# Performance work log

Measured on AMD Instinct MI355X. Metric: run time of the kernel, lower is better.

The kernel has to match this reference:

```python
import jax, jax.numpy as jnp
import numpy as np

N = 50000      # nodes
E = 800000     # edges (before self loops)
IN = 128       # in_channels
HID = 64       # hidden_channels
HEADS = 4
NCLS = 2
NEG_SLOPE = 0.2
BN_EPS = 1e-5

# per-layer config: (in_dim, heads, out_c, concat)
LAYERS = [(IN, HEADS, HID, True), (HID*HEADS, HEADS, HID, True), (HID*HEADS, HEADS, HID, True), (HID*HEADS, 1, HID, False)]

def setup_inputs():
    key = jax.random.key(0)
    ks = iter(jax.random.split(key, 64))
    d = {}
    d['x'] = jax.random.normal(next(ks), (N, IN), dtype=jnp.float32)
    d['edge_index'] = jax.random.randint(next(ks), (2, E), 0, N, dtype=jnp.int64)
    for i, (inc, h, oc, concat) in enumerate(LAYERS):
        d[f'W{i}'] = jax.random.normal(next(ks), (inc, h*oc), dtype=jnp.float32) * (1.0/np.sqrt(inc))
        d[f'as{i}'] = jax.random.normal(next(ks), (h, oc), dtype=jnp.float32) * 0.1
        d[f'ad{i}'] = jax.random.normal(next(ks), (h, oc), dtype=jnp.float32) * 0.1
        bn_dim = h*oc if concat else oc
        d[f'b{i}'] = jnp.zeros((bn_dim,), dtype=jnp.float32)
        d[f'g{i}'] = jnp.ones((bn_dim,), dtype=jnp.float32)
        d[f'be{i}'] = jnp.zeros((bn_dim,), dtype=jnp.float32)
    d['hw1'] = jax.random.normal(next(ks), (HID, HID//2), dtype=jnp.float32) * (1.0/np.sqrt(HID))
    d['hb1'] = jnp.zeros((HID//2,), dtype=jnp.float32)
    d['hw2'] = jax.random.normal(next(ks), (HID//2, NCLS), dtype=jnp.float32) * (1.0/np.sqrt(HID//2))
    d['hb2'] = jnp.zeros((NCLS,), dtype=jnp.float32)
    return d

def _gat_layer(x, src, dst, W, a_src, a_dst, bias, heads, out_c, concat):
    n = x.shape[0]
    h = (x @ W).reshape(n, heads, out_c)                 # [N,H,C]
    asrc = jnp.einsum('nhc,hc->nh', h, a_src)            # [N,H]
    adst = jnp.einsum('nhc,hc->nh', h, a_dst)            # [N,H]
    e = asrc[src] + adst[dst]                            # [Etot,H]
    e = jax.nn.leaky_relu(e, NEG_SLOPE)
    # segment softmax over incoming edges of each dst node
    m = jax.ops.segment_max(e, dst, num_segments=n)
    m = jnp.where(jnp.isfinite(m), m, 0.0)
    ex = jnp.exp(e - m[dst])
    s = jax.ops.segment_sum(ex, dst, num_segments=n)
    alpha = ex / (s[dst] + 1e-16)                        # [Etot,H]
    msg = h[src] * alpha[:, :, None]                     # [Etot,H,C]
    out = jax.ops.segment_sum(msg, dst, num_segments=n)  # [N,H,C]
    out = out.reshape(n, heads*out_c) if concat else out.mean(axis=1)
    return out + bias

def _bn(x, g, b):
    mu = x.mean(axis=0)
    var = x.var(axis=0)
    return g * (x - mu) * jax.lax.rsqrt(var + BN_EPS) + b

def reference(x, edge_index,
              W0, as0, ad0, b0, g0, be0,
              W1, as1, ad1, b1, g1, be1,
              W2, as2, ad2, b2, g2, be2,
              W3, as3, ad3, b3, g3, be3,
              hw1, hb1, hw2, hb2):
    loop = jnp.arange(N, dtype=edge_index.dtype)
    src = jnp.concatenate([edge_index[0], loop])
    dst = jnp.concatenate([edge_index[1], loop])
    params = [(W0, as0, ad0, b0, g0, be0), (W1, as1, ad1, b1, g1, be1),
              (W2, as2, ad2, b2, g2, be2), (W3, as3, ad3, b3, g3, be3)]
    h = x
    for (inc, heads, oc, concat), (W, a_s, a_d, b, g, be) in zip(LAYERS, params):
        h = _gat_layer(h, src, dst, W, a_s, a_d, b, heads, oc, concat)
        h = _bn(h, g, be)
        h = jax.nn.relu(h)
    h = jax.nn.relu(h @ hw1 + hb1)
    return h @ hw2 + hb2
```

## Files before the change

kernel.cpp:

```cpp
#include <hip/hip_runtime.h>

__device__ __forceinline__ float bf2f(unsigned short u) {
    union { unsigned int i; float f; } x;
    x.i = ((unsigned int)u) << 16;
    return x.f;
}
__device__ __forceinline__ unsigned short f2bf(float f) {
    union { float f; unsigned int i; } x;
    x.f = f;
    unsigned int r = x.i + 0x7fffu + ((x.i >> 16) & 1u);
    return (unsigned short)(r >> 16);
}
__device__ __forceinline__ float ldf(const void* p, int i, int f32m) {
    if (f32m) return ((const float*)p)[i];
    return bf2f(((const unsigned short*)p)[i]);
}
__device__ __forceinline__ void unpack2(unsigned int u, float& lo, float& hi) {
    union { unsigned int i; float f; } a, b;
    a.i = u << 16;
    b.i = u & 0xffff0000u;
    lo = a.f;
    hi = b.f;
}

__global__ void GATModel_20117626814707_kernel(unsigned short* out, int n) {
    int i = blockIdx.x * 256 + threadIdx.x;
    if (i < n) out[i] = f2bf(100.0f);
}

__global__ void zero_kernel(int* p, int n) {
    int i = blockIdx.x * 256 + threadIdx.x;
    if (i < n) p[i] = 0;
}

__global__ void probe_kernel(const int* ei, const unsigned int* xw, int* meta) {
    if (threadIdx.x == 0 && blockIdx.x == 0) {
        int orv = 0;
        for (int k = 0; k < 64; k++) orv |= ei[2 * k + 1];
        meta[0] = (orv == 0) ? 1 : 0;
        int cnt = 0;
        for (int k = 0; k < 64; k++) {
            unsigned int w = xw[k];
            int e = (int)((w >> 23) & 0xffu);
            if (e >= 107 && e <= 140) cnt++;
        }
        meta[1] = (cnt >= 48) ? 1 : 0;
    }
}

__global__ void hist_kernel(const int* ei, const int* meta, int* cnt, int E, int N) {
    int e = blockIdx.x * 256 + threadIdx.x;
    if (e >= E) return;
    int d = meta[0] ? ei[2 * (E + e)] : ei[E + e];
    if ((unsigned)d >= (unsigned)N) d = 0;
    atomicAdd(&cnt[d], 1);
}

__global__ void __launch_bounds__(1024) scan_kernel(const int* cnt, int* offs, int N) {
    __shared__ int part[1024];
    int tid = threadIdx.x;
    int per = (N + 1023) >> 10;
    int b = tid * per;
    int e_ = b + per;
    if (e_ > N) e_ = N;
    if (b > N) b = N;
    int s = 0;
    for (int i = b; i < e_; i++) s += cnt[i];
    part[tid] = s;
    __syncthreads();
    for (int off = 1; off < 1024; off <<= 1) {
        int t = (tid >= off) ? part[tid - off] : 0;
        __syncthreads();
        part[tid] += t;
        __syncthreads();
    }
    int run = part[tid] - s;
    for (int i = b; i < e_; i++) { offs[i] = run; run += cnt[i]; }
    if (tid == 1023) offs[N] = part[1023];
}

__global__ void scatter_kernel(const int* ei, const int* meta, const int* offs,
                               int* fill, int* csr, int E, int N) {
    int e = blockIdx.x * 256 + threadIdx.x;
    if (e >= E) return;
    int is64 = meta[0];
    int sv = is64 ? ei[2 * e] : ei[e];
    int d  = is64 ? ei[2 * (E + e)] : ei[E + e];
    if ((unsigned)sv >= (unsigned)N) sv = 0;
    if ((unsigned)d  >= (unsigned)N) d  = 0;
    int pos = offs[d] + atomicAdd(&fill[d], 1);
    csr[pos] = sv;
}

__global__ void __launch_bounds__(256) gemm_tiled(const void* Aptr, int a_is_input,
                                                  const void* Bptr, void* Cout, int out_bf16,
                                                  const void* aw_s, const void* aw_d,
                                                  float* asrc, float* adst,
                                                  int M, int K, int NC, const int* meta,
                                                  const float* bnscale, const float* bnshift,
                                                  int apply_bn) {
    __shared__ float At[32][68];
    __shared__ float Bt[32][64];
    int wmode = meta[1];
    int amode = a_is_input ? wmode : 1;
    int t = threadIdx.x;
    int row0 = blockIdx.x * 64;
    int col0 = blockIdx.y * 64;
    int H = NC >> 6;

    int tx = t & 15;
    int ty = t >> 4;

    int ar = t >> 2;
    int ak = (t & 3) * 8;
    int bk = t >> 3;
    int bc = (t & 7) * 8;

    float acc[4][4];
    #pragma unroll
    for (int i = 0; i < 4; i++)
        #pragma unroll
        for (int j = 0; j < 4; j++) acc[i][j] = 0.0f;

    for (int kt = 0; kt < K; kt += 32) {
        {
            int gr = row0 + ar;
            float av[8];
            if (gr < M) {
                if (amode) {
                    const float* ap = (const float*)Aptr + (size_t)gr * K + kt + ak;
                    float4 v0 = *(const float4*)ap;
                    float4 v1 = *(const float4*)(ap + 4);
                    av[0] = v0.x; av[1] = v0.y; av[2] = v0.z; av[3] = v0.w;
                    av[4] = v1.x; av[5] = v1.y; av[6] = v1.z; av[7] = v1.w;
                    if (apply_bn) {
                        float4 sc0 = *(const float4*)(bnscale + kt + ak);
                        float4 sc1 = *(const float4*)(bnscale + kt + ak + 4);
                        float4 sh0 = *(const float4*)(bnshift + kt + ak);
                        float4 sh1 = *(const float4*)(bnshift + kt + ak + 4);
                        av[0] = fmaxf(fmaf(av[0], sc0.x, sh0.x), 0.0f);
                        av[1] = fmaxf(fmaf(av[1], sc0.y, sh0.y), 0.0f);
                        av[2] = fmaxf(fmaf(av[2], sc0.z, sh0.z), 0.0f);
                        av[3] = fmaxf(fmaf(av[3], sc0.w, sh0.w), 0.0f);
                        av[4] = fmaxf(fmaf(av[4], sc1.x, sh1.x), 0.0f);
                        av[5] = fmaxf(fmaf(av[5], sc1.y, sh1.y), 0.0f);
                        av[6] = fmaxf(fmaf(av[6], sc1.z, sh1.z), 0.0f);
                        av[7] = fmaxf(fmaf(av[7], sc1.w, sh1.w), 0.0f);
                    }
                } else {
                    const unsigned short* ap =
                        (const unsigned short*)Aptr + (size_t)gr * K + kt + ak;
                    uint4 u = *(const uint4*)ap;
                    unpack2(u.x, av[0], av[1]);
                    unpack2(u.y, av[2], av[3]);
                    unpack2(u.z, av[4], av[5]);
                    unpack2(u.w, av[6], av[7]);
                }
            } else {
                #pragma unroll
                for (int i = 0; i < 8; i++) av[i] = 0.0f;
            }
            #pragma unroll
            for (int i = 0; i < 8; i++) At[ak + i][ar] = av[i];
        }
        {
            if (wmode) {
                const float* bp = (const float*)Bptr + (size_t)(kt + bk) * NC + col0 + bc;
                *(float4*)&Bt[bk][bc] = *(const float4*)bp;
                *(float4*)&Bt[bk][bc + 4] = *(const float4*)(bp + 4);
            } else {
                const unsigned short* bp =
                    (const unsigned short*)Bptr + (size_t)(kt + bk) * NC + col0 + bc;
                uint4 u = *(const uint4*)bp;
                float4 v0, v1;
                unpack2(u.x, v0.x, v0.y);
                unpack2(u.y, v0.z, v0.w);
                unpack2(u.z, v1.x, v1.y);
                unpack2(u.w, v1.z, v1.w);
                *(float4*)&Bt[bk][bc] = v0;
                *(float4*)&Bt[bk][bc + 4] = v1;
            }
        }
        __syncthreads();

        #pragma unroll
        for (int k = 0; k < 32; k++) {
            float4 a = *(float4*)&At[k][ty * 4];
            float4 b = *(float4*)&Bt[k][tx * 4];
            acc[0][0] = fmaf(a.x, b.x, acc[0][0]);
            acc[0][1] = fmaf(a.x, b.y, acc[0][1]);
            acc[0][2] = fmaf(a.x, b.z, acc[0][2]);
            acc[0][3] = fmaf(a.x, b.w, acc[0][3]);
            acc[1][0] = fmaf(a.y, b.x, acc[1][0]);
            acc[1][1] = fmaf(a.y, b.y, acc[1][1]);
            acc[1][2] = fmaf(a.y, b.z, acc[1][2]);
            acc[1][3] = fmaf(a.y, b.w, acc[1][3]);
            acc[2][0] = fmaf(a.z, b.x, acc[2][0]);
            acc[2][1] = fmaf(a.z, b.y, acc[2][1]);
            acc[2][2] = fmaf(a.z, b.z, acc[2][2]);
            acc[2][3] = fmaf(a.z, b.w, acc[2][3]);
            acc[3][0] = fmaf(a.w, b.x, acc[3][0]);
            acc[3][1] = fmaf(a.w, b.y, acc[3][1]);
            acc[3][2] = fmaf(a.w, b.z, acc[3][2]);
            acc[3][3] = fmaf(a.w, b.w, acc[3][3]);
        }
        __syncthreads();
    }

    #pragma unroll
    for (int i = 0; i < 4; i++) {
        int gr = row0 + ty * 4 + i;
        if (gr < M) {
            if (out_bf16) {
                uint2 v;
                v.x = (unsigned int)f2bf(acc[i][0]) | ((unsigned int)f2bf(acc[i][1]) << 16);
                v.y = (unsigned int)f2bf(acc[i][2]) | ((unsigned int)f2bf(acc[i][3]) << 16);
                *(uint2*)&((unsigned short*)Cout)[(size_t)gr * NC + col0 + tx * 4] = v;
            } else {
                float4 v;
                v.x = acc[i][0]; v.y = acc[i][1]; v.z = acc[i][2]; v.w = acc[i][3];
                *(float4*)&((float*)Cout)[(size_t)gr * NC + col0 + tx * 4] = v;
            }
        }
    }

    int ai = blockIdx.y * 64 + tx * 4;
    float as0 = ldf(aw_s, ai + 0, wmode), as1 = ldf(aw_s, ai + 1, wmode);
    float as2 = ldf(aw_s, ai + 2, wmode), as3 = ldf(aw_s, ai + 3, wmode);
    float ad0 = ldf(aw_d, ai + 0, wmode), ad1 = ldf(aw_d, ai + 1, wmode);
    float ad2 = ldf(aw_d, ai + 2, wmode), ad3 = ldf(aw_d, ai + 3, wmode);
    #pragma unroll
    for (int i = 0; i < 4; i++) {
        float ps = acc[i][0] * as0 + acc[i][1] * as1 + acc[i][2] * as2 + acc[i][3] * as3;
        float pd = acc[i][0] * ad0 + acc[i][1] * ad1 + acc[i][2] * ad2 + acc[i][3] * ad3;
        #pragma unroll
        for (int off = 1; off < 16; off <<= 1) {
            ps += __shfl_xor(ps, off);
            pd += __shfl_xor(pd, off);
        }
        int gr = row0 + ty * 4 + i;
        if (tx == 0 && gr < M) {
            asrc[gr * H + blockIdx.y] = ps;
            adst[gr * H + blockIdx.y] = pd;
        }
    }
}

__global__ void __launch_bounds__(256) aggb4(const unsigned short* hfb, const float* asrc,
                                             const float* adst, const int* offs,
                                             const int* csr, float* out, int N) {
    int wid = threadIdx.x >> 6;
    int l = threadIdx.x & 63;
    int node = blockIdx.x * 4 + wid;
    if (node >= N) return;
    int h = l >> 4;
    int beg = offs[node], end = offs[node + 1];
    float ad = adst[node * 4 + h];
    float e0 = asrc[node * 4 + h] + ad;
    e0 = (e0 < 0.0f) ? 0.2f * e0 : e0;
    float w0 = __expf(e0);
    uint2 u0 = ((const uint2*)(hfb + (size_t)node * 256))[l];
    float g0a, g0b, g0c, g0d;
    unpack2(u0.x, g0a, g0b);
    unpack2(u0.y, g0c, g0d);
    float s = w0;
    float a0 = w0 * g0a, a1 = w0 * g0b, a2 = w0 * g0c, a3 = w0 * g0d;
    int i = beg;
    for (; i + 4 <= end; i += 4) {
        int s0 = csr[i], s1 = csr[i + 1], s2 = csr[i + 2], s3 = csr[i + 3];
        float e_0 = asrc[s0 * 4 + h] + ad;
        float e_1 = asrc[s1 * 4 + h] + ad;
        float e_2 = asrc[s2 * 4 + h] + ad;
        float e_3 = asrc[s3 * 4 + h] + ad;
        uint2 u_0 = ((const uint2*)(hfb + (size_t)s0 * 256))[l];
        uint2 u_1 = ((const uint2*)(hfb + (size_t)s1 * 256))[l];
        uint2 u_2 = ((const uint2*)(hfb + (size_t)s2 * 256))[l];
        uint2 u_3 = ((const uint2*)(hfb + (size_t)s3 * 256))[l];
        e_0 = (e_0 < 0.0f) ? 0.2f * e_0 : e_0;
        e_1 = (e_1 < 0.0f) ? 0.2f * e_1 : e_1;
        e_2 = (e_2 < 0.0f) ? 0.2f * e_2 : e_2;
        e_3 = (e_3 < 0.0f) ? 0.2f * e_3 : e_3;
        float wv0 = __expf(e_0), wv1 = __expf(e_1), wv2 = __expf(e_2), wv3 = __expf(e_3);
        s += (wv0 + wv1) + (wv2 + wv3);
        float x0, x1, x2, x3;
        unpack2(u_0.x, x0, x1); unpack2(u_0.y, x2, x3);
        a0 = fmaf(wv0, x0, a0); a1 = fmaf(wv0, x1, a1);
        a2 = fmaf(wv0, x2, a2); a3 = fmaf(wv0, x3, a3);
        unpack2(u_1.x, x0, x1); unpack2(u_1.y, x2, x3);
        a0 = fmaf(wv1, x0, a0); a1 = fmaf(wv1, x1, a1);
        a2 = fmaf(wv1, x2, a2); a3 = fmaf(wv1, x3, a3);
        unpack2(u_2.x, x0, x1); unpack2(u_2.y, x2, x3);
        a0 = fmaf(wv2, x0, a0); a1 = fmaf(wv2, x1, a1);
        a2 = fmaf(wv2, x2, a2); a3 = fmaf(wv2, x3, a3);
        unpack2(u_3.x, x0, x1); unpack2(u_3.y, x2, x3);
        a0 = fmaf(wv3, x0, a0); a1 = fmaf(wv3, x1, a1);
        a2 = fmaf(wv3, x2, a2); a3 = fmaf(wv3, x3, a3);
    }
    for (; i < end; i++) {
        int sn = csr[i];
        float es = asrc[sn * 4 + h] + ad;
        es = (es < 0.0f) ? 0.2f * es : es;
        float wv = __expf(es);
        uint2 u = ((const uint2*)(hfb + (size_t)sn * 256))[l];
        float x0, x1, x2, x3;
        unpack2(u.x, x0, x1); unpack2(u.y, x2, x3);
        s += wv;
        a0 = fmaf(wv, x0, a0); a1 = fmaf(wv, x1, a1);
        a2 = fmaf(wv, x2, a2); a3 = fmaf(wv, x3, a3);
    }
    float rs = 1.0f / (s + 1e-16f);
    float4 o;
    o.x = a0 * rs; o.y = a1 * rs; o.z = a2 * rs; o.w = a3 * rs;
    *(float4*)&out[(size_t)node * 256 + l * 4] = o;
}

__global__ void __launch_bounds__(256) aggf1(const float* hf, const float* asrc,
                                             const float* adst, const int* offs,
                                             const int* csr, float* out, int N) {
    int wid = threadIdx.x >> 6;
    int c = threadIdx.x & 63;
    int node = blockIdx.x * 4 + wid;
    if (node >= N) return;
    int beg = offs[node], end = offs[node + 1];
    float ad = adst[node];
    float e0 = asrc[node] + ad;
    e0 = (e0 < 0.0f) ? 0.2f * e0 : e0;
    float w0 = __expf(e0);
    float s = w0;
    float acc0 = w0 * hf[(size_t)node * 64 + c];
    float acc1 = 0.0f, acc2 = 0.0f, acc3 = 0.0f;
    int i = beg;
    for (; i + 4 <= end; i += 4) {
        int s0 = csr[i], s1 = csr[i + 1], s2 = csr[i + 2], s3 = csr[i + 3];
        float e_0 = asrc[s0] + ad;
        float e_1 = asrc[s1] + ad;
        float e_2 = asrc[s2] + ad;
        float e_3 = asrc[s3] + ad;
        float g0 = hf[(size_t)s0 * 64 + c];
        float g1 = hf[(size_t)s1 * 64 + c];
        float g2 = hf[(size_t)s2 * 64 + c];
        float g3 = hf[(size_t)s3 * 64 + c];
        e_0 = (e_0 < 0.0f) ? 0.2f * e_0 : e_0;
        e_1 = (e_1 < 0.0f) ? 0.2f * e_1 : e_1;
        e_2 = (e_2 < 0.0f) ? 0.2f * e_2 : e_2;
        e_3 = (e_3 < 0.0f) ? 0.2f * e_3 : e_3;
        float w0_ = __expf(e_0), w1_ = __expf(e_1), w2_ = __expf(e_2), w3_ = __expf(e_3);
        s += (w0_ + w1_) + (w2_ + w3_);
        acc0 = fmaf(w0_, g0, acc0);
        acc1 = fmaf(w1_, g1, acc1);
        acc2 = fmaf(w2_, g2, acc2);
        acc3 = fmaf(w3_, g3, acc3);
    }
    for (; i < end; i++) {
        int sn = csr[i];
        float es = asrc[sn] + ad;
        es = (es < 0.0f) ? 0.2f * es : es;
        float wv = __expf(es);
        s += wv;
        acc0 = fmaf(wv, hf[(size_t)sn * 64 + c], acc0);
    }
    float acc = (acc0 + acc1) + (acc2 + acc3);
    out[(size_t)node * 64 + c] = acc / (s + 1e-16f);
}

__global__ void __launch_bounds__(256) bnstats_kernel(const float* x, float* sum, float* sq,
                                                      int N, int NC, int ncshift) {
    int f = threadIdx.x & (NC - 1);
    int rsub = threadIdx.x >> ncshift;
    int rstep = 256 >> ncshift;
    int r0 = blockIdx.x * 256 + rsub;
    int r1 = blockIdx.x * 256 + 256;
    if (r1 > N) r1 = N;
    float s = 0.0f, q = 0.0f;
    for (int r = r0; r < r1; r += rstep) {
        float v = x[(size_t)r * NC + f];
        s += v;
        q += v * v;
    }
    atomicAdd(&sum[f], s);
    atomicAdd(&sq[f], q);
}

__global__ void bnfinal(const float* sum, const float* sq, const void* g, const void* be,
                        float* scale, float* shift, int NC, float invN, const int* meta) {
    int f = threadIdx.x;
    if (f >= NC) return;
    int wmode = meta[1];
    float mu = sum[f] * invN;
    float var = sq[f] * invN - mu * mu;
    if (var < 0.0f) var = 0.0f;
    float rs = rsqrtf(var + 1e-5f);
    float sc = ldf(g, f, wmode) * rs;
    scale[f] = sc;
    shift[f] = ldf(be, f, wmode) - mu * sc;
}

__global__ void __launch_bounds__(256) head_kernel(const float* xin, const float* bnscale,
                                                   const float* bnshift, const void* hw1,
                                                   const void* hb1, const void* hw2,
                                                   const void* hb2, void* out, int N,
                                                   const int* meta) {
    __shared__ float w1[64 * 32];
    __shared__ float w2[64];
    __shared__ float b1[32];
    __shared__ float b2[2];
    __shared__ float sc[64];
    __shared__ float sh[64];
    int wmode = meta[1];
    for (int i = threadIdx.x; i < 2048; i += 256) w1[i] = ldf(hw1, i, wmode);
    if (threadIdx.x < 64) {
        w2[threadIdx.x] = ldf(hw2, threadIdx.x, wmode);
        sc[threadIdx.x] = bnscale[threadIdx.x];
        sh[threadIdx.x] = bnshift[threadIdx.x];
    }
    if (threadIdx.x < 32) b1[threadIdx.x] = ldf(hb1, threadIdx.x, wmode);
    if (threadIdx.x < 2) b2[threadIdx.x] = ldf(hb2, threadIdx.x, wmode);
    __syncthreads();
    int n = blockIdx.x * 256 + threadIdx.x;
    if (n >= N) return;
    float x[64];
    for (int i = 0; i < 64; i++)
        x[i] = fmaxf(fmaf(xin[(size_t)n * 64 + i], sc[i], sh[i]), 0.0f);
    float o0 = b2[0], o1 = b2[1];
    for (int j = 0; j < 32; j++) {
        float a = b1[j];
        #pragma unroll
        for (int k = 0; k < 64; k++) a = fmaf(x[k], w1[k * 32 + j], a);
        a = fmaxf(a, 0.0f);
        o0 = fmaf(a, w2[j * 2], o0);
        o1 = fmaf(a, w2[j * 2 + 1], o1);
    }
    if (wmode) {
        ((float*)out)[n * 2] = o0;
        ((float*)out)[n * 2 + 1] = o1;
    } else {
        ((unsigned short*)out)[n * 2] = f2bf(o0);
        ((unsigned short*)out)[n * 2 + 1] = f2bf(o1);
    }
}

extern "C" void kernel_launch(void* const* d_in, const int* in_sizes, int n_in,
                              void* d_out, int out_size, void* d_ws, size_t ws_size,
                              hipStream_t stream) {
    unsigned short* outp = (unsigned short*)d_out;
    size_t out_bytes2 = (size_t)out_size * 2;
    int gOut = (out_size + 255) / 256;

    GATModel_20117626814707_kernel<<<gOut, 256, 0, stream>>>(outp, out_size);

    if (n_in != 30 || in_sizes[0] != 50000 * 128 || in_sizes[1] != 2 * 800000 ||
        in_sizes[2] != 128 * 256 || in_sizes[26] != 64 * 32) {
        hipMemsetAsync(d_out, 0x4E, out_bytes2, stream);
        return;
    }

    const int N = 50000;
    const int E = 800000;

    const void* x_in = d_in[0];
    const int* ei = (const int*)d_in[1];
    const void* W0  = d_in[2];
    const void* As0 = d_in[3];
    const void* Ad0 = d_in[4];
    const void* G0  = d_in[6];
    const void* Be0 = d_in[7];
    const void* W1  = d_in[8];
    const void* As1 = d_in[9];
    const void* Ad1 = d_in[10];
    const void* G1  = d_in[12];
    const void* Be1 = d_in[13];
    const void* W2  = d_in[14];
    const void* As2 = d_in[15];
    const void* Ad2 = d_in[16];
    const void* G2  = d_in[18];
    const void* Be2 = d_in[19];
    const void* W3  = d_in[20];
    const void* As3 = d_in[21];
    const void* Ad3 = d_in[22];
    const void* G3  = d_in[24];
    const void* Be3 = d_in[25];
    const void* hw1 = d_in[26];
    const void* hb1 = d_in[27];
    const void* hw2 = d_in[28];
    const void* hb2 = d_in[29];

    char* base = (char*)d_ws;
    size_t off = 0;
    auto alloc = [&](size_t bytes) {
        void* r = (void*)(base + off);
        off += (bytes + 255) & ~(size_t)255;
        return r;
    };
    int* meta    = (int*)alloc(256);
    int* cnt     = (int*)alloc((size_t)N * 4);
    int* fill    = (int*)alloc((size_t)N * 4);
    float* stats = (float*)alloc(4 * 2 * 256 * 4);
    size_t zero_end = off;
    int* offs    = (int*)alloc((size_t)(N + 1) * 4);
    int* csr     = (int*)alloc((size_t)E * 4);
    float* asrc  = (float*)alloc((size_t)N * 4 * 4);
    float* adst  = (float*)alloc((size_t)N * 4 * 4);
    float* scaleb = (float*)alloc(256 * 4);
    float* shiftb = (float*)alloc(256 * 4);
    unsigned short* hfb = (unsigned short*)alloc((size_t)N * 256 * 2);
    float* hff   = (float*)alloc((size_t)N * 64 * 4);
    float* xbuf  = (float*)alloc((size_t)N * 256 * 4);

    if (ws_size < off) {
        hipMemsetAsync(d_out, 0x4D, out_bytes2, stream);
        return;
    }

    int zn = (int)((zero_end - 256) / 4);
    zero_kernel<<<(zn + 255) / 256, 256, 0, stream>>>(cnt, zn);
    probe_kernel<<<1, 64, 0, stream>>>(ei, (const unsigned int*)x_in, meta);

    int gE = (E + 255) / 256;
    hist_kernel<<<gE, 256, 0, stream>>>(ei, meta, cnt, E, N);
    scan_kernel<<<1, 1024, 0, stream>>>(cnt, offs, N);
    scatter_kernel<<<gE, 256, 0, stream>>>(ei, meta, offs, fill, csr, E, N);

    int gM64 = (N + 63) / 64;
    int gBN = (N + 255) / 256;
    int gND = (N + 3) / 4;
    float invN = 1.0f / (float)N;

    const void* Wl[3]  = {W0, W1, W2};
    const void* Asl[3] = {As0, As1, As2};
    const void* Adl[3] = {Ad0, Ad1, Ad2};
    const void* Gl[3]  = {G0, G1, G2};
    const void* Bel[3] = {Be0, Be1, Be2};
    for (int L = 0; L < 3; L++) {
        if (L == 0)
            gemm_tiled<<<dim3(gM64, 4), 256, 0, stream>>>(
                x_in, 1, Wl[L], hfb, 1, Asl[L], Adl[L], asrc, adst, N, 128, 256, meta,
                scaleb, shiftb, 0);
        else
            gemm_tiled<<<dim3(gM64, 4), 256, 0, stream>>>(
                xbuf, 0, Wl[L], hfb, 1, Asl[L], Adl[L], asrc, adst, N, 256, 256, meta,
                scaleb, shiftb, 1);
        aggb4<<<gND, 256, 0, stream>>>(hfb, asrc, adst, offs, csr, xbuf, N);
        bnstats_kernel<<<gBN, 256, 0, stream>>>(xbuf, stats + L * 512, stats + L * 512 + 256, N, 256, 8);
        bnfinal<<<1, 256, 0, stream>>>(stats + L * 512, stats + L * 512 + 256, Gl[L], Bel[L],
                                       scaleb, shiftb, 256, invN, meta);
    }

    gemm_tiled<<<dim3(gM64, 1), 256, 0, stream>>>(
        xbuf, 0, W3, hff, 0, As3, Ad3, asrc, adst, N, 256, 64, meta, scaleb, shiftb, 1);
    aggf1<<<gND, 256, 0, stream>>>(hff, asrc, adst, offs, csr, xbuf, N);
    bnstats_kernel<<<gBN, 256, 0, stream>>>(xbuf, stats + 1536, stats + 1792, N, 64, 6);
    bnfinal<<<1, 256, 0, stream>>>(stats + 1536, stats + 1792, G3, Be3,
                                   scaleb, shiftb, 64, invN, meta);

    head_kernel<<<gBN, 256, 0, stream>>>(xbuf, scaleb, shiftb, hw1, hb1, hw2, hb2, d_out, N, meta);
}
```

Measured before the change: 1.075 ms.

## Replace FP32 SIMT GEMM with split-bf16 MFMA GEMM using hi/lo operand decomposition

The FP32 FMA tiled GEMM is replaced by a matrix-core kernel using bf16 MFMA 16x16x32 instructions. Accuracy is kept close to FP32 by splitting each operand into high and low bf16 parts and issuing three MFMAs (hi*hi, lo*hi, hi*lo). New pre-pass kernels split the activations, with BN+ReLU fused in, and transpose-split the weights. This adds extra memory passes for the split activation buffers and three MFMAs per tile.

```diff
diff --git a/kernel.cpp b/kernel.cpp
--- a/kernel.cpp
+++ b/kernel.cpp
@@ -1,4 +1,7 @@
 #include <hip/hip_runtime.h>
+
+typedef __attribute__((ext_vector_type(8))) short bf16x8;
+typedef __attribute__((ext_vector_type(4))) float f32x4;
 
 __device__ __forceinline__ float bf2f(unsigned short u) {
     union { unsigned int i; float f; } x;
@@ -92,156 +95,161 @@
     csr[pos] = sv;
 }
 
-__global__ void __launch_bounds__(256) gemm_tiled(const void* Aptr, int a_is_input,
-                                                  const void* Bptr, void* Cout, int out_bf16,
-                                                  const void* aw_s, const void* aw_d,
-                                                  float* asrc, float* adst,
-                                                  int M, int K, int NC, const int* meta,
-                                                  const float* bnscale, const float* bnshift,
-                                                  int apply_bn) {
-    __shared__ float At[32][68];
-    __shared__ float Bt[32][64];
+__global__ void __launch_bounds__(256) split_kernel(const void* X, int x_is_input,
+                                                    const int* meta, const float* scale,
+                                                    const float* shift, int apply_bn,
+                                                    unsigned short* hi, unsigned short* lo,
+                                                    int total4, int kmask) {
+    int idx = blockIdx.x * 256 + threadIdx.x;
+    if (idx >= total4) return;
+    int base = idx * 4;
+    int xmode = x_is_input ? meta[1] : 1;
+    float v[4];
+    if (xmode) {
+        float4 f = *(const float4*)((const float*)X + base);
+        v[0] = f.x; v[1] = f.y; v[2] = f.z; v[3] = f.w;
+    } else {
+        uint2 u = *(const uint2*)((const unsigned short*)X + base);
+        unpack2(u.x, v[0], v[1]);
+        unpack2(u.y, v[2], v[3]);
+    }
+    if (apply_bn) {
+        int f0 = base & kmask;
+        #pragma unroll
+        for (int j = 0; j < 4; j++)
+            v[j] = fmaxf(fmaf(v[j], scale[f0 + j], shift[f0 + j]), 0.0f);
+    }
+    unsigned short h[4], l[4];
+    #pragma unroll
+    for (int j = 0; j < 4; j++) {
+        h[j] = f2bf(v[j]);
+        l[j] = f2bf(v[j] - bf2f(h[j]));
+    }
+    uint2 ho, loo;
+    ho.x = (unsigned int)h[0] | ((unsigned int)h[1] << 16);
+    ho.y = (unsigned int)h[2] | ((unsigned int)h[3] << 16);
+    loo.x = (unsigned int)l[0] | ((unsigned int)l[1] << 16);
+    loo.y = (unsigned int)l[2] | ((unsigned int)l[3] << 16);
+    *(uint2*)(hi + base) = ho;
+    *(uint2*)(lo + base) = loo;
+}
+
+__global__ void __launch_bounds__(256) wsplit_kernel(const void* W, const int* meta,
+                                                     unsigned short* hiT, unsigned short* loT,
+                                                     int K, int ncshift, int total) {
+    int e = blockIdx.x * 256 + threadIdx.x;
+    if (e >= total) return;
+    int k = e >> ncshift;
+    int n = e & ((1 << ncshift) - 1);
+    float x = ldf(W, e, meta[1]);
+    unsigned short h = f2bf(x);
+    hiT[n * K + k] = h;
+    loT[n * K + k] = f2bf(x - bf2f(h));
+}
+
+__global__ void __launch_bounds__(256) gemm_mfma(const unsigned short* Ahi,
+                                                 const unsigned short* Alo,
+                                                 const unsigned short* Bhi,
+                                                 const unsigned short* Blo,
+                                                 void* Cout, int out_bf16,
+                                                 const void* aw_s, const void* aw_d,
+                                                 float* asrc, float* adst,
+                                                 int M, int K, int NC, const int* meta) {
+    __shared__ unsigned short sAhi[64 * 40];
+    __shared__ unsigned short sAlo[64 * 40];
+    __shared__ unsigned short sBhi[64 * 40];
+    __shared__ unsigned short sBlo[64 * 40];
     int wmode = meta[1];
-    int amode = a_is_input ? wmode : 1;
     int t = threadIdx.x;
+    int wid = t >> 6;
+    int lane = t & 63;
     int row0 = blockIdx.x * 64;
     int col0 = blockIdx.y * 64;
     int H = NC >> 6;
 
-    int tx = t & 15;
-    int ty = t >> 4;
-
     int ar = t >> 2;
     int ak = (t & 3) * 8;
-    int bk = t >> 3;
-    int bc = (t & 7) * 8;
-
-    float acc[4][4];
+
+    f32x4 acc[4];
     #pragma unroll
-    for (int i = 0; i < 4; i++)
-        #pragma unroll
-        for (int j = 0; j < 4; j++) acc[i][j] = 0.0f;
+    for (int i = 0; i < 4; i++) acc[i] = (f32x4){0.0f, 0.0f, 0.0f, 0.0f};
+
+    int m = lane & 15;
+    int q = lane >> 4;
 
     for (int kt = 0; kt < K; kt += 32) {
         {
             int gr = row0 + ar;
-            float av[8];
+            uint4 h4 = {0, 0, 0, 0}, l4 = {0, 0, 0, 0};
             if (gr < M) {
-                if (amode) {
-                    const float* ap = (const float*)Aptr + (size_t)gr * K + kt + ak;
-                    float4 v0 = *(const float4*)ap;
-                    float4 v1 = *(const float4*)(ap + 4);
-                    av[0] = v0.x; av[1] = v0.y; av[2] = v0.z; av[3] = v0.w;
-                    av[4] = v1.x; av[5] = v1.y; av[6] = v1.z; av[7] = v1.w;
-                    if (apply_bn) {
-                        float4 sc0 = *(const float4*)(bnscale + kt + ak);
-                        float4 sc1 = *(const float4*)(bnscale + kt + ak + 4);
-                        float4 sh0 = *(const float4*)(bnshift + kt + ak);
-                        float4 sh1 = *(const float4*)(bnshift + kt + ak + 4);
-                        av[0] = fmaxf(fmaf(av[0], sc0.x, sh0.x), 0.0f);
-                        av[1] = fmaxf(fmaf(av[1], sc0.y, sh0.y), 0.0f);
-                        av[2] = fmaxf(fmaf(av[2], sc0.z, sh0.z), 0.0f);
-                        av[3] = fmaxf(fmaf(av[3], sc0.w, sh0.w), 0.0f);
-                        av[4] = fmaxf(fmaf(av[4], sc1.x, sh1.x), 0.0f);
-                        av[5] = fmaxf(fmaf(av[5], sc1.y, sh1.y), 0.0f);
-                        av[6] = fmaxf(fmaf(av[6], sc1.z, sh1.z), 0.0f);
-                        av[7] = fmaxf(fmaf(av[7], sc1.w, sh1.w), 0.0f);
-                    }
-                } else {
-                    const unsigned short* ap =
-                        (const unsigned short*)Aptr + (size_t)gr * K + kt + ak;
-                    uint4 u = *(const uint4*)ap;
-                    unpack2(u.x, av[0], av[1]);
-                    unpack2(u.y, av[2], av[3]);
-                    unpack2(u.z, av[4], av[5]);
-                    unpack2(u.w, av[6], av[7]);
-                }
-            } else {
-                #pragma unroll
-                for (int i = 0; i < 8; i++) av[i] = 0.0f;
+                h4 = *(const uint4*)(Ahi + (size_t)gr * K + kt + ak);
+                l4 = *(const uint4*)(Alo + (size_t)gr * K + kt + ak);
             }
-            #pragma unroll
-            for (int i = 0; i < 8; i++) At[ak + i][ar] = av[i];
-        }
-        {
-            if (wmode) {
-                const float* bp = (const float*)Bptr + (size_t)(kt + bk) * NC + col0 + bc;
-                *(float4*)&Bt[bk][bc] = *(const float4*)bp;
-                *(float4*)&Bt[bk][bc + 4] = *(const float4*)(bp + 4);
-            } else {
-                const unsigned short* bp =
-                    (const unsigned short*)Bptr + (size_t)(kt + bk) * NC + col0 + bc;
-                uint4 u = *(const uint4*)bp;
-                float4 v0, v1;
-                unpack2(u.x, v0.x, v0.y);
-                unpack2(u.y, v0.z, v0.w);
-                unpack2(u.z, v1.x, v1.y);
-                unpack2(u.w, v1.z, v1.w);
-                *(float4*)&Bt[bk][bc] = v0;
-                *(float4*)&Bt[bk][bc + 4] = v1;
+            *(uint4*)(sAhi + ar * 40 + ak) = h4;
+            *(uint4*)(sAlo + ar * 40 + ak) = l4;
+            uint4 bh4 = *(const uint4*)(Bhi + (size_t)(col0 + ar) * K + kt + ak);
+            uint4 bl4 = *(const uint4*)(Blo + (size_t)(col0 + ar) * K + kt + ak);
+            *(uint4*)(sBhi + ar * 40 + ak) = bh4;
+            *(uint4*)(sBlo + ar * 40 + ak) = bl4;
+        }
+        __syncthreads();
+
+        bf16x8 ahi = *(const bf16x8*)(sAhi + (wid * 16 + m) * 40 + q * 8);
+        bf16x8 alo = *(const bf16x8*)(sAlo + (wid * 16 + m) * 40 + q * 8);
+        #pragma unroll
+        for (int tn = 0; tn < 4; tn++) {
+            bf16x8 bhi = *(const bf16x8*)(sBhi + (tn * 16 + m) * 40 + q * 8);
+            bf16x8 blo = *(const bf16x8*)(sBlo + (tn * 16 + m) * 40 + q * 8);
+            acc[tn] = __builtin_amdgcn_mfma_f32_16x16x32_bf16(ahi, bhi, acc[tn], 0, 0, 0);
+            acc[tn] = __builtin_amdgcn_mfma_f32_16x16x32_bf16(alo, bhi, acc[tn], 0, 0, 0);
+            acc[tn] = __builtin_amdgcn_mfma_f32_16x16x32_bf16(ahi, blo, acc[tn], 0, 0, 0);
+        }
+        __syncthreads();
+    }
+
+    #pragma unroll
+    for (int tn = 0; tn < 4; tn++) {
+        int gcol = col0 + tn * 16 + m;
+        #pragma unroll
+        for (int reg = 0; reg < 4; reg++) {
+            int grow = row0 + wid * 16 + q * 4 + reg;
+            if (grow < M) {
+                if (out_bf16)
+                    ((unsigned short*)Cout)[(size_t)grow * NC + gcol] = f2bf(acc[tn][reg]);
+                else
+                    ((float*)Cout)[(size_t)grow * NC + gcol] = acc[tn][reg];
             }
         }
-        __syncthreads();
-
-        #pragma unroll
-        for (int k = 0; k < 32; k++) {
-            float4 a = *(float4*)&At[k][ty * 4];
-            float4 b = *(float4*)&Bt[k][tx * 4];
-            acc[0][0] = fmaf(a.x, b.x, acc[0][0]);
-            acc[0][1] = fmaf(a.x, b.y, acc[0][1]);
-            acc[0][2] = fmaf(a.x, b.z, acc[0][2]);
-            acc[0][3] = fmaf(a.x, b.w, acc[0][3]);
-            acc[1][0] = fmaf(a.y, b.x, acc[1][0]);
-            acc[1][1] = fmaf(a.y, b.y, acc[1][1]);
-            acc[1][2] = fmaf(a.y, b.z, acc[1][2]);
-            acc[1][3] = fmaf(a.y, b.w, acc[1][3]);
-            acc[2][0] = fmaf(a.z, b.x, acc[2][0]);
-            acc[2][1] = fmaf(a.z, b.y, acc[2][1]);
-            acc[2][2] = fmaf(a.z, b.z, acc[2][2]);
-            acc[2][3] = fmaf(a.z, b.w, acc[2][3]);
-            acc[3][0] = fmaf(a.w, b.x, acc[3][0]);
-            acc[3][1] = fmaf(a.w, b.y, acc[3][1]);
-            acc[3][2] = fmaf(a.w, b.z, acc[3][2]);
-            acc[3][3] = fmaf(a.w, b.w, acc[3][3]);
-        }
-        __syncthreads();
-    }
-
+    }
+
+    float ps[4] = {0.f, 0.f, 0.f, 0.f};
+    float pd[4] = {0.f, 0.f, 0.f, 0.f};
     #pragma unroll
-    for (int i = 0; i < 4; i++) {
-        int gr = row0 + ty * 4 + i;
-        if (gr < M) {
-            if (out_bf16) {
-                uint2 v;
-                v.x = (unsigned int)f2bf(acc[i][0]) | ((unsigned int)f2bf(acc[i][1]) << 16);
-                v.y = (unsigned int)f2bf(acc[i][2]) | ((unsigned int)f2bf(acc[i][3]) << 16);
-                *(uint2*)&((unsigned short*)Cout)[(size_t)gr * NC + col0 + tx * 4] = v;
-            } else {
-                float4 v;
-                v.x = acc[i][0]; v.y = acc[i][1]; v.z = acc[i][2]; v.w = acc[i][3];
-                *(float4*)&((float*)Cout)[(size_t)gr * NC + col0 + tx * 4] = v;
+    for (int tn = 0; tn < 4; tn++) {
+        float asv = ldf(aw_s, blockIdx.y * 64 + tn * 16 + m, wmode);
+        float adv = ldf(aw_d, blockIdx.y * 64 + tn * 16 + m, wmode);
+        #pragma unroll
+        for (int reg = 0; reg < 4; reg++) {
+            ps[reg] = fmaf(acc[tn][reg], asv, ps[reg]);
+            pd[reg] = fmaf(acc[tn][reg], adv, pd[reg]);
+        }
+    }
+    #pragma unroll
+    for (int reg = 0; reg < 4; reg++) {
+        #pragma unroll
+        for (int off = 1; off < 16; off <<= 1) {
+            ps[reg] += __shfl_xor(ps[reg], off);
+            pd[reg] += __shfl_xor(pd[reg], off);
+        }
+    }
+    if (m == 0) {
+        #pragma unroll
+        for (int reg = 0; reg < 4; reg++) {
+            int grow = row0 + wid * 16 + q * 4 + reg;
+            if (grow < M) {
+                asrc[grow * H + blockIdx.y] = ps[reg];
+                adst[grow * H + blockIdx.y] = pd[reg];
             }
-        }
-    }
-
-    int ai = blockIdx.y * 64 + tx * 4;
-    float as0 = ldf(aw_s, ai + 0, wmode), as1 = ldf(aw_s, ai + 1, wmode);
-    float as2 = ldf(aw_s, ai + 2, wmode), as3 = ldf(aw_s, ai + 3, wmode);
-    float ad0 = ldf(aw_d, ai + 0, wmode), ad1 = ldf(aw_d, ai + 1, wmode);
-    float ad2 = ldf(aw_d, ai + 2, wmode), ad3 = ldf(aw_d, ai + 3, wmode);
-    #pragma unroll
-    for (int i = 0; i < 4; i++) {
-        float ps = acc[i][0] * as0 + acc[i][1] * as1 + acc[i][2] * as2 + acc[i][3] * as3;
-        float pd = acc[i][0] * ad0 + acc[i][1] * ad1 + acc[i][2] * ad2 + acc[i][3] * ad3;
-        #pragma unroll
-        for (int off = 1; off < 16; off <<= 1) {
-            ps += __shfl_xor(ps, off);
-            pd += __shfl_xor(pd, off);
-        }
-        int gr = row0 + ty * 4 + i;
-        if (tx == 0 && gr < M) {
-            asrc[gr * H + blockIdx.y] = ps;
-            adst[gr * H + blockIdx.y] = pd;
         }
     }
 }
@@ -505,6 +513,16 @@
     unsigned short* hfb = (unsigned short*)alloc((size_t)N * 256 * 2);
     float* hff   = (float*)alloc((size_t)N * 64 * 4);
     float* xbuf  = (float*)alloc((size_t)N * 256 * 4);
+    unsigned short* ahi = (unsigned short*)alloc((size_t)N * 256 * 2);
+    unsigned short* alo = (unsigned short*)alloc((size_t)N * 256 * 2);
+    unsigned short* w0hi = (unsigned short*)alloc(128 * 256 * 2);
+    unsigned short* w0lo = (unsigned short*)alloc(128 * 256 * 2);
+    unsigned short* w1hi = (unsigned short*)alloc(256 * 256 * 2);
+    unsigned short* w1lo = (unsigned short*)alloc(256 * 256 * 2);
+    unsigned short* w2hi = (unsigned short*)alloc(256 * 256 * 2);
+    unsigned short* w2lo = (unsigned short*)alloc(256 * 256 * 2);
+    unsigned short* w3hi = (unsigned short*)alloc(256 * 64 * 2);
+    unsigned short* w3lo = (unsigned short*)alloc(256 * 64 * 2);
 
     if (ws_size < off) {
         hipMemsetAsync(d_out, 0x4D, out_bytes2, stream);
@@ -520,33 +538,43 @@
     scan_kernel<<<1, 1024, 0, stream>>>(cnt, offs, N);
     scatter_kernel<<<gE, 256, 0, stream>>>(ei, meta, offs, fill, csr, E, N);
 
+    wsplit_kernel<<<(128 * 256 + 255) / 256, 256, 0, stream>>>(W0, meta, w0hi, w0lo, 128, 8, 128 * 256);
+    wsplit_kernel<<<(256 * 256 + 255) / 256, 256, 0, stream>>>(W1, meta, w1hi, w1lo, 256, 8, 256 * 256);
+    wsplit_kernel<<<(256 * 256 + 255) / 256, 256, 0, stream>>>(W2, meta, w2hi, w2lo, 256, 8, 256 * 256);
+    wsplit_kernel<<<(256 * 64 + 255) / 256, 256, 0, stream>>>(W3, meta, w3hi, w3lo, 256, 6, 256 * 64);
+
     int gM64 = (N + 63) / 64;
     int gBN = (N + 255) / 256;
     int gND = (N + 3) / 4;
     float invN = 1.0f / (float)N;
 
-    const void* Wl[3]  = {W0, W1, W2};
-    const void* Asl[3] = {As0, As1, As2};
-    const void* Adl[3] = {Ad0, Ad1, Ad2};
-    const void* Gl[3]  = {G0, G1, G2};
-    const void* Bel[3] = {Be0, Be1, Be2};
+    const unsigned short* whi[4] = {w0hi, w1hi, w2hi, w3hi};
+    const unsigned short* wlo[4] = {w0lo, w1lo, w2lo, w3lo};
+    const void* Asl[4] = {As0, As1, As2, As3};
+    const void* Adl[4] = {Ad0, Ad1, Ad2, Ad3};
+    const void* Gl[4]  = {G0, G1, G2, G3};
+    const void* Bel[4] = {Be0, Be1, Be2, Be3};
+
     for (int L = 0; L < 3; L++) {
         if (L == 0)
-            gemm_tiled<<<dim3(gM64, 4), 256, 0, stream>>>(
-                x_in, 1, Wl[L], hfb, 1, Asl[L], Adl[L], asrc, adst, N, 128, 256, meta,
-                scaleb, shiftb, 0);
+            split_kernel<<<(N * 128 / 4 + 255) / 256, 256, 0, stream>>>(
+                x_in, 1, meta, scaleb, shiftb, 0, ahi, alo, N * 128 / 4, 127);
         else
-            gemm_tiled<<<dim3(gM64, 4), 256, 0, stream>>>(
-                xbuf, 0, Wl[L], hfb, 1, Asl[L], Adl[L], asrc, adst, N, 256, 256, meta,
-                scaleb, shiftb, 1);
+            split_kernel<<<(N * 256 / 4 + 255) / 256, 256, 0, stream>>>(
+                xbuf, 0, meta, scaleb, shiftb, 1, ahi, alo, N * 256 / 4, 255);
+        int K = (L == 0) ? 128 : 256;
+        gemm_mfma<<<dim3(gM64, 4), 256, 0, stream>>>(
+            ahi, alo, whi[L], wlo[L], hfb, 1, Asl[L], Adl[L], asrc, adst, N, K, 256, meta);
         aggb4<<<gND, 256, 0, stream>>>(hfb, asrc, adst, offs, csr, xbuf, N);
         bnstats_kernel<<<gBN, 256, 0, stream>>>(xbuf, stats + L * 512, stats + L * 512 + 256, N, 256, 8);
         bnfinal<<<1, 256, 0, stream>>>(stats + L * 512, stats + L * 512 + 256, Gl[L], Bel[L],
                                        scaleb, shiftb, 256, invN, meta);
     }
 
-    gemm_tiled<<<dim3(gM64, 1), 256, 0, stream>>>(
-        xbuf, 0, W3, hff, 0, As3, Ad3, asrc, adst, N, 256, 64, meta, scaleb, shiftb, 1);
+    split_kernel<<<(N * 256 / 4 + 255) / 256, 256, 0, stream>>>(
+        xbuf, 0, meta, scaleb, shiftb, 1, ahi, alo, N * 256 / 4, 255);
+    gemm_mfma<<<dim3(gM64, 1), 256, 0, stream>>>(
+        ahi, alo, w3hi, w3lo, hff, 0, As3, Ad3, asrc, adst, N, 256, 64, meta);
     aggf1<<<gND, 256, 0, stream>>>(hff, asrc, adst, offs, csr, xbuf, N);
     bnstats_kernel<<<gBN, 256, 0, stream>>>(xbuf, stats + 1536, stats + 1792, N, 64, 6);
     bnfinal<<<1, 256, 0, stream>>>(stats + 1536, stats + 1792, G3, Be3,
```

Result: faster. 998.4 us (-7.1%).
